# Optimization experiments

Hardware: AMD Instinct MI355X
Metric: run time of the kernel (lower is better)

Reference implementation:

```python
import jax, jax.numpy as jnp
import numpy as np

N_SITES = 4096
NUM_TYPES = 3
INTERACTION_ORDER = 4
BATCH = 64


def _make_symmetric(t):
    # symmetrize over the two type axes (alpha, beta)
    return (t + jnp.transpose(t, (1, 0, 2))) / 2.0


def setup_inputs() -> dict:
    key = jax.random.key(0)
    k1, k2, k3 = jax.random.split(key, 3)
    interaction = _make_symmetric(
        jax.random.uniform(k1, (NUM_TYPES, NUM_TYPES, INTERACTION_ORDER), dtype=jnp.float32)
    )
    adjacency = jax.random.uniform(
        k2, (N_SITES, N_SITES, INTERACTION_ORDER), dtype=jnp.float32
    )
    v_batch = jax.random.normal(k3, (N_SITES, NUM_TYPES, BATCH), dtype=jnp.float32)
    return {
        "interaction_tensor": interaction,
        "adjacency_tensor": adjacency,
        "v_batch": v_batch,
    }


def reference(interaction_tensor, adjacency_tensor, v_batch):
    # E_s = 0.5 * sum_{a,b,n,i,j} W[a,b,n] * A[i,j,n] * v[i,a,s] * v[j,b,s]
    # Contract the big adjacency against v first so the (i,j,a,b) intermediate
    # is never materialized: A(ijn) x v(jbs) -> t(inbs) is the only O(N^2) step.
    t = jnp.einsum('ijn,jbs->inbs', adjacency_tensor, v_batch)  # [N, n, T, S]
    out = 0.5 * jnp.einsum('inbs,ias,abn->s', t, v_batch, interaction_tensor)
    return out
```

## Files before the change

### kernel.cpp

```cpp
#include <hip/hip_runtime.h>
#include <hip/hip_bf16.h>


typedef __attribute__((ext_vector_type(8))) short short8;
typedef __attribute__((ext_vector_type(4))) float floatx4;

#define VF_U4 (12*512*16)
#define NBLK  512

__device__ __forceinline__ unsigned short f2bf(float f) {
    union { float f; unsigned u; } x; x.f = f;
    unsigned r = x.u + 0x7fffu + ((x.u >> 16) & 1u);
    return (unsigned short)(r >> 16);
}
__device__ __forceinline__ unsigned pack2(float lo, float hi) {
    return (unsigned)f2bf(lo) | ((unsigned)f2bf(hi) << 16);
}

__global__ void prep_vfrag(const float* __restrict__ v, uint4* __restrict__ vf) {
    int tid = blockIdx.x * 256 + threadIdx.x;
    if (tid >= VF_U4) return;
    int ci = tid & 15;
    int kb = (tid >> 4) & 511;
    int f  = tid >> 13;
    int c = f * 16 + ci;
    int b = c >> 6, s = c & 63;
    int j0 = kb * 8;
    unsigned q0 = pack2(v[((j0+0)*3+b)*64+s], v[((j0+1)*3+b)*64+s]);
    unsigned q1 = pack2(v[((j0+2)*3+b)*64+s], v[((j0+3)*3+b)*64+s]);
    unsigned q2 = pack2(v[((j0+4)*3+b)*64+s], v[((j0+5)*3+b)*64+s]);
    unsigned q3 = pack2(v[((j0+6)*3+b)*64+s], v[((j0+7)*3+b)*64+s]);
    vf[tid] = make_uint4(q0, q1, q2, q3);
}

__global__ __launch_bounds__(512, 2) void energy_main(
        const float* __restrict__ A, const float* __restrict__ v,
        const float* __restrict__ W, const uint4* __restrict__ vf,
        float* __restrict__ partials) {
    __shared__ __align__(16) unsigned As32[4096];
    __shared__ float Wl[36];
    __shared__ float El[64];

    const int tid = threadIdx.x;
    const int bid = blockIdx.x;
    const int ib = bid >> 1, jh = bid & 1;
    const int i0 = ib * 16;
    const int jbase = jh * 2048;

    if (tid < 36) Wl[tid] = W[tid];
    if (tid < 64) El[tid] = 0.0f;

    const int lane = tid & 63;
    const int w = tid >> 6;
    const int kh = w >> 2;
    const int ws = w & 3;

    const int r  = tid >> 5;
    const int jp = tid & 31;
    const long arowBase = (long)(i0 + r) * 4096 + jbase + 2 * jp;
    const int aWrIdx = r * 32 + (((jp >> 2) ^ (r & 7)) << 2) + (jp & 3);

    const int rr = lane & 15;
    const int gA = (kh * 4 + (lane >> 4)) ^ (rr & 7);
    const int aRdOff = rr * 128 + gA * 16;

    const int kbBase = (jbase + kh * 32) >> 3;

    floatx4 acc[4][3];
    #pragma unroll
    for (int n = 0; n < 4; ++n)
        #pragma unroll
        for (int cf = 0; cf < 3; ++cf)
            #pragma unroll
            for (int q = 0; q < 4; ++q) acc[n][cf][q] = 0.0f;

    const floatx4* A4 = reinterpret_cast<const floatx4*>(A);

    {
        floatx4 a0 = A4[arowBase];
        floatx4 a1 = A4[arowBase + 1];
        As32[0*512 + aWrIdx] = pack2(a0.x, a1.x);
        As32[1*512 + aWrIdx] = pack2(a0.y, a1.y);
        As32[2*512 + aWrIdx] = pack2(a0.z, a1.z);
        As32[3*512 + aWrIdx] = pack2(a0.w, a1.w);
    }
    short8 bc[3];
    #pragma unroll
    for (int cf = 0; cf < 3; ++cf)
        bc[cf] = *reinterpret_cast<const short8*>(vf + ((ws*3+cf)*512 + kbBase)*16 + lane);

    int cur = 0;
    for (int t = 0; t < 32; ++t) {
        __syncthreads();
        floatx4 na0, na1;
        short8 bn[3];
        if (t < 31) {
            long o = arowBase + (long)(t + 1) * 64;
            na0 = A4[o];
            na1 = A4[o + 1];
            int kb = kbBase + (t + 1) * 8;
            #pragma unroll
            for (int cf = 0; cf < 3; ++cf)
                bn[cf] = *reinterpret_cast<const short8*>(vf + ((ws*3+cf)*512 + kb)*16 + lane);
        }
        const char* ab = reinterpret_cast<const char*>(As32) + cur * 8192 + aRdOff;
        short8 af[4];
        #pragma unroll
        for (int n = 0; n < 4; ++n)
            af[n] = *reinterpret_cast<const short8*>(ab + n * 2048);
        #pragma unroll
        for (int n = 0; n < 4; ++n)
            #pragma unroll
            for (int cf = 0; cf < 3; ++cf)
                acc[n][cf] = __builtin_amdgcn_mfma_f32_16x16x32_bf16(
                    af[n], bc[cf], acc[n][cf], 0, 0, 0);
        __syncthreads();
        if (t < 31) {
            const int base = (cur ^ 1) * 2048 + aWrIdx;
            As32[base + 0*512] = pack2(na0.x, na1.x);
            As32[base + 1*512] = pack2(na0.y, na1.y);
            As32[base + 2*512] = pack2(na0.z, na1.z);
            As32[base + 3*512] = pack2(na0.w, na1.w);
            bc[0] = bn[0]; bc[1] = bn[1]; bc[2] = bn[2];
        }
        cur ^= 1;
    }

    float cont[3];
    #pragma unroll
    for (int cf = 0; cf < 3; ++cf) {
        int c = ws * 48 + cf * 16 + rr;
        int b = c >> 6, s = c & 63;
        float sum = 0.0f;
        #pragma unroll
        for (int rg = 0; rg < 4; ++rg) {
            int i = i0 + (lane >> 4) * 4 + rg;
            float v0 = v[(i * 3 + 0) * 64 + s];
            float v1 = v[(i * 3 + 1) * 64 + s];
            float v2 = v[(i * 3 + 2) * 64 + s];
            #pragma unroll
            for (int n = 0; n < 4; ++n) {
                float P = Wl[b * 4 + n] * v0 + Wl[12 + b * 4 + n] * v1
                        + Wl[24 + b * 4 + n] * v2;
                sum += acc[n][cf][rg] * P;
            }
        }
        cont[cf] = sum;
    }
    #pragma unroll
    for (int cf = 0; cf < 3; ++cf) {
        cont[cf] += __shfl_xor(cont[cf], 16);
        cont[cf] += __shfl_xor(cont[cf], 32);
    }
    __syncthreads();
    if (lane < 16) {
        #pragma unroll
        for (int cf = 0; cf < 3; ++cf) {
            int s = (ws * 48 + cf * 16 + lane) & 63;
            atomicAdd(&El[s], cont[cf]);
        }
    }
    __syncthreads();
    if (tid < 64) partials[bid * 64 + tid] = 0.5f * El[tid];
}

__global__ void reduce_out(const float* __restrict__ partials, float* __restrict__ out) {
    __shared__ float red[8][64];
    int tid = threadIdx.x;
    int chunk = tid >> 6, s = tid & 63;
    float a = 0.0f;
    for (int m = 0; m < NBLK / 8; ++m)
        a += partials[((m << 3) + chunk) * 64 + s];
    red[chunk][s] = a;
    __syncthreads();
    if (tid < 64) {
        float t = 0.0f;
        #pragma unroll
        for (int c = 0; c < 8; ++c) t += red[c][tid];
        out[tid] = t;
    }
}

extern "C" void kernel_launch(void* const* d_in, const int* in_sizes, int n_in,
                              void* d_out, int out_size, void* d_ws, size_t ws_size,
                              hipStream_t stream) {
    const float* W = (const float*)d_in[0];
    const float* A = (const float*)d_in[1];
    const float* v = (const float*)d_in[2];
    float* out = (float*)d_out;
    uint4* vf = (uint4*)d_ws;
    float* partials = (float*)((char*)d_ws + (size_t)VF_U4 * 16);

    hipLaunchKernelGGL(prep_vfrag, dim3((VF_U4 + 255) / 256), dim3(256), 0, stream, v, vf);
    hipLaunchKernelGGL(energy_main, dim3(NBLK), dim3(512), 0, stream, A, v, W, vf, partials);
    hipLaunchKernelGGL(reduce_out, dim3(1), dim3(512), 0, stream, partials, out);
}
```

Baseline: 68.86 us.

## Double K-tile depth per iteration, halving loop trips and barriers

Each iteration now stages 128 columns of A per row instead of 64, so every thread loads four float4s and writes packed uint2 pairs into a larger double-buffered LDS tile with a wider XOR swizzle. The loop runs 16 times instead of 32, and each pass does two MFMA K-chunks, which halves the barrier count and raises the number of global loads in flight. The vf B fragments are now loaded inside the loop rather than prefetched a step ahead. LDS use doubles to 32 KB per block, which may affect the two-blocks-per-CU occupancy, and the unprefetched B loads may stall the MFMAs.

```diff
diff --git a/kernel.cpp b/kernel.cpp
--- a/kernel.cpp
+++ b/kernel.cpp
@@ -37,7 +37,7 @@
         const float* __restrict__ A, const float* __restrict__ v,
         const float* __restrict__ W, const uint4* __restrict__ vf,
         float* __restrict__ partials) {
-    __shared__ __align__(16) unsigned As32[4096];
+    __shared__ __align__(16) unsigned As32[8192];
     __shared__ float Wl[36];
     __shared__ float El[64];
 
@@ -57,14 +57,14 @@
 
     const int r  = tid >> 5;
     const int jp = tid & 31;
-    const long arowBase = (long)(i0 + r) * 4096 + jbase + 2 * jp;
-    const int aWrIdx = r * 32 + (((jp >> 2) ^ (r & 7)) << 2) + (jp & 3);
+    const long arowBase = (long)(i0 + r) * 4096 + jbase + 4 * jp;
+    const int aWrIdx = r * 64 + (((jp >> 1) ^ (r & 15)) << 2) + ((jp & 1) << 1);
 
     const int rr = lane & 15;
-    const int gA = (kh * 4 + (lane >> 4)) ^ (rr & 7);
-    const int aRdOff = rr * 128 + gA * 16;
-
-    const int kbBase = (jbase + kh * 32) >> 3;
+    const int g4 = lane >> 4;
+    const int aRdRow = rr * 256;
+
+    const int kbBase = (jbase >> 3) + kh * 8;
 
     floatx4 acc[4][3];
     #pragma unroll
@@ -77,51 +77,58 @@
     const floatx4* A4 = reinterpret_cast<const floatx4*>(A);
 
     {
-        floatx4 a0 = A4[arowBase];
-        floatx4 a1 = A4[arowBase + 1];
-        As32[0*512 + aWrIdx] = pack2(a0.x, a1.x);
-        As32[1*512 + aWrIdx] = pack2(a0.y, a1.y);
-        As32[2*512 + aWrIdx] = pack2(a0.z, a1.z);
-        As32[3*512 + aWrIdx] = pack2(a0.w, a1.w);
-    }
-    short8 bc[3];
-    #pragma unroll
-    for (int cf = 0; cf < 3; ++cf)
-        bc[cf] = *reinterpret_cast<const short8*>(vf + ((ws*3+cf)*512 + kbBase)*16 + lane);
+        floatx4 na[4];
+        #pragma unroll
+        for (int q = 0; q < 4; ++q) na[q] = A4[arowBase + q];
+        #pragma unroll
+        for (int n = 0; n < 4; ++n) {
+            uint2 w2 = make_uint2(pack2(na[0][n], na[1][n]),
+                                  pack2(na[2][n], na[3][n]));
+            *reinterpret_cast<uint2*>(&As32[n * 1024 + aWrIdx]) = w2;
+        }
+    }
 
     int cur = 0;
-    for (int t = 0; t < 32; ++t) {
+    for (int t = 0; t < 16; ++t) {
         __syncthreads();
-        floatx4 na0, na1;
-        short8 bn[3];
-        if (t < 31) {
-            long o = arowBase + (long)(t + 1) * 64;
-            na0 = A4[o];
-            na1 = A4[o + 1];
-            int kb = kbBase + (t + 1) * 8;
-            #pragma unroll
-            for (int cf = 0; cf < 3; ++cf)
-                bn[cf] = *reinterpret_cast<const short8*>(vf + ((ws*3+cf)*512 + kb)*16 + lane);
-        }
-        const char* ab = reinterpret_cast<const char*>(As32) + cur * 8192 + aRdOff;
-        short8 af[4];
-        #pragma unroll
-        for (int n = 0; n < 4; ++n)
-            af[n] = *reinterpret_cast<const short8*>(ab + n * 2048);
-        #pragma unroll
-        for (int n = 0; n < 4; ++n)
-            #pragma unroll
-            for (int cf = 0; cf < 3; ++cf)
-                acc[n][cf] = __builtin_amdgcn_mfma_f32_16x16x32_bf16(
-                    af[n], bc[cf], acc[n][cf], 0, 0, 0);
+        floatx4 na[4];
+        if (t < 15) {
+            long o = arowBase + (long)(t + 1) * 128;
+            #pragma unroll
+            for (int q = 0; q < 4; ++q) na[q] = A4[o + q];
+        }
+        const char* abase = reinterpret_cast<const char*>(As32) + cur * 16384;
+        #pragma unroll
+        for (int kc = 0; kc < 2; ++kc) {
+            short8 bc[3];
+            #pragma unroll
+            for (int cf = 0; cf < 3; ++cf) {
+                int kb = kbBase + kc * 4 + t * 16;
+                bc[cf] = *reinterpret_cast<const short8*>(
+                    vf + ((ws * 3 + cf) * 512 + kb) * 16 + lane);
+            }
+            short8 af[4];
+            const int gOff = (((kh << 3) + (kc << 2) + g4) ^ (rr & 15)) << 4;
+            #pragma unroll
+            for (int n = 0; n < 4; ++n)
+                af[n] = *reinterpret_cast<const short8*>(
+                    abase + n * 4096 + aRdRow + gOff);
+            #pragma unroll
+            for (int n = 0; n < 4; ++n)
+                #pragma unroll
+                for (int cf = 0; cf < 3; ++cf)
+                    acc[n][cf] = __builtin_amdgcn_mfma_f32_16x16x32_bf16(
+                        af[n], bc[cf], acc[n][cf], 0, 0, 0);
+        }
         __syncthreads();
-        if (t < 31) {
-            const int base = (cur ^ 1) * 2048 + aWrIdx;
-            As32[base + 0*512] = pack2(na0.x, na1.x);
-            As32[base + 1*512] = pack2(na0.y, na1.y);
-            As32[base + 2*512] = pack2(na0.z, na1.z);
-            As32[base + 3*512] = pack2(na0.w, na1.w);
-            bc[0] = bn[0]; bc[1] = bn[1]; bc[2] = bn[2];
+        if (t < 15) {
+            unsigned* dst = &As32[(cur ^ 1) * 4096];
+            #pragma unroll
+            for (int n = 0; n < 4; ++n) {
+                uint2 w2 = make_uint2(pack2(na[0][n], na[1][n]),
+                                      pack2(na[2][n], na[3][n]));
+                *reinterpret_cast<uint2*>(&dst[n * 1024 + aWrIdx]) = w2;
+            }
         }
         cur ^= 1;
     }
```

New measurement: 93.58 us. +35.9%, slower.
